# Kernel tuning notes

Measured on AMD Instinct MI355X. Metric: run time of the kernel, lower is better.

Reference implementation:

```python
import math
import jax, jax.numpy as jnp
import numpy as np

MODEL_DIM = 2048
NUM_EXPERTS = 64
NUM_TOKENS = 8192
CAPACITY_FACTOR = 1.0


def setup_inputs() -> dict:
    key = jax.random.key(0)
    kx, kw = jax.random.split(key)
    x = jax.random.normal(kx, (NUM_TOKENS, MODEL_DIM), dtype=jnp.float32)
    # Linear(model_dim, num_experts, bias=False): weight [E, D], y = x @ W.T
    wg = jax.random.normal(kw, (NUM_EXPERTS, MODEL_DIM), dtype=jnp.float32) * (1.0 / math.sqrt(MODEL_DIM))
    return {"x": x, "wg": wg}


def reference(x, wg):
    # ---- gate projection: logits [S, E] ----
    logits = jnp.einsum('sd,ed->se', x, wg)
    gates = jax.nn.softmax(logits, axis=1)
    S, E = gates.shape
    # training mode -> capacity = capacity_factor * ceil(S / E)  (static)
    capacity = int(CAPACITY_FACTOR * math.ceil(S / E))

    # ---- top-1 expert selection ----
    indices1_s = jnp.argmax(gates, axis=1)                      # [S]
    mask1 = jax.nn.one_hot(indices1_s, E, dtype=jnp.int32)      # [S, E]

    # gate value of the chosen expert per token
    gates1_s = jnp.sum(gates * mask1.astype(gates.dtype), axis=1)  # [S]

    # position of each token within its expert's queue (cumsum over tokens)
    locations1 = jnp.cumsum(mask1, axis=0) - 1                  # [S, E]

    # ---- load-balancing auxiliary loss ----
    me = jnp.mean(gates, axis=0)                                # [E]
    ce = jnp.mean(mask1.astype(gates.dtype), axis=0)            # [E]
    l_aux = jnp.mean(me * ce) * (E * E)

    # ---- capacity enforcement: drop tokens beyond expert capacity ----
    mask1 = mask1 * (locations1 < capacity).astype(mask1.dtype) # [S, E]
    locations1_s = jnp.sum(locations1 * mask1, axis=1)          # [S]

    # ---- combine / dispatch tensors ----
    gates1 = gates1_s[:, None] * mask1.astype(gates.dtype)      # [S, E]
    locations1_sc = jax.nn.one_hot(locations1_s, capacity, dtype=gates.dtype)  # [S, C]
    # torch.bmm(gates1[:, :, None], locations1_sc[:, None, :]) == outer product per token
    combine1_sec = jnp.einsum('se,sc->sec', gates1, locations1_sc)  # [S, E, C]
    dispatch_mask = combine1_sec > 0                            # bool [S, E, C]

    return l_aux, combine1_sec, dispatch_mask
```

## Files before the change

kernel.cpp:

```cpp
#include <hip/hip_runtime.h>
#include <math.h>

#define NUM_TOK 8192
#define DIM     2048
#define NEXP    64
#define CAP     128

#define TM      32
#define BK      64
#define NT      256
#define NBLKA   (NUM_TOK/TM)
#define NCHUNK  (DIM/BK)

#define XS_STR  72
#define WS_STR  68
#define LG_STR  (NEXP+1)

#define ZFLT    524288u
#define ZPER    (ZFLT/NCHUNK)

__global__ __launch_bounds__(NT) void gate_fused(
    const float* __restrict__ x, const float* __restrict__ wg,
    float* __restrict__ out,
    int* __restrict__ expert_idx, float* __restrict__ gate_top,
    float* __restrict__ me_partial, int* __restrict__ counts)
{
    __shared__ __align__(16) float xs[TM * XS_STR];
    __shared__ __align__(16) float wss[BK * WS_STR];
    __shared__ __align__(16) float logits_s[TM * LG_STR];
    __shared__ float me_s[NEXP];
    __shared__ int   cnt_s[NEXP];

    const int tid = threadIdx.x;
    const int bid = blockIdx.x;
    const int tx  = tid & 15;
    const int ty  = tid >> 4;
    const int tok0 = bid * TM;

    if (tid < NEXP) { me_s[tid] = 0.0f; cnt_s[tid] = 0; }

    float acc[2][4] = {};

    float* zbase = out + 1 + (size_t)bid * ZFLT;
    const float4 z4 = make_float4(0.f, 0.f, 0.f, 0.f);

    for (int kc = 0; kc < NCHUNK; ++kc) {
        const int k0 = kc * BK;

        {
            float4* zp = (float4*)(zbase + (size_t)kc * ZPER) + tid;
            #pragma unroll
            for (int q = 0; q < 16; ++q) zp[q * NT] = z4;
        }

        #pragma unroll
        for (int q = 0; q < 2; ++q) {
            int id = tid + NT * q;
            int r = id >> 4, cf = id & 15;
            float4 v = *(const float4*)(x + (size_t)(tok0 + r) * DIM + k0 + 4 * cf);
            *(float4*)(&xs[r * XS_STR + 4 * cf]) = v;
        }
        {
            int cf = tid & 15, er = tid >> 4;
            #pragma unroll
            for (int i = 0; i < 4; ++i) {
                int e = er + 16 * i;
                float4 v = *(const float4*)(wg + (size_t)e * DIM + k0 + 4 * cf);
                wss[(4 * cf + 0) * WS_STR + e] = v.x;
                wss[(4 * cf + 1) * WS_STR + e] = v.y;
                wss[(4 * cf + 2) * WS_STR + e] = v.z;
                wss[(4 * cf + 3) * WS_STR + e] = v.w;
            }
        }
        __syncthreads();

        #pragma unroll
        for (int kk = 0; kk < BK; kk += 4) {
            float4 xa = *(const float4*)(&xs[(2 * ty + 0) * XS_STR + kk]);
            float4 xb = *(const float4*)(&xs[(2 * ty + 1) * XS_STR + kk]);
            #pragma unroll
            for (int j = 0; j < 4; ++j) {
                float4 w = *(const float4*)(&wss[(kk + j) * WS_STR + 4 * tx]);
                float xaj = (&xa.x)[j], xbj = (&xb.x)[j];
                acc[0][0] += xaj * w.x; acc[0][1] += xaj * w.y;
                acc[0][2] += xaj * w.z; acc[0][3] += xaj * w.w;
                acc[1][0] += xbj * w.x; acc[1][1] += xbj * w.y;
                acc[1][2] += xbj * w.z; acc[1][3] += xbj * w.w;
            }
        }
        __syncthreads();
    }

    #pragma unroll
    for (int i = 0; i < 2; ++i)
        #pragma unroll
        for (int j = 0; j < 4; ++j)
            logits_s[(2 * ty + i) * LG_STR + 4 * tx + j] = acc[i][j];
    __syncthreads();

    const int lane = tid & 63;
    const int wv   = tid >> 6;
    float me_acc = 0.0f;
    for (int r8 = 0; r8 < 8; ++r8) {
        int row = wv * 8 + r8;
        float v = logits_s[row * LG_STR + lane];
        float m = v; int mi = lane;
        #pragma unroll
        for (int off = 32; off > 0; off >>= 1) {
            float om = __shfl_xor(m, off);
            int  omi = __shfl_xor(mi, off);
            if (om > m || (om == m && omi < mi)) { m = om; mi = omi; }
        }
        float ex = __expf(v - m);
        float s = ex;
        #pragma unroll
        for (int off = 32; off > 0; off >>= 1) s += __shfl_xor(s, off);
        me_acc += ex / s;
        if (lane == mi) {
            int token = tok0 + row;
            expert_idx[token] = mi;
            gate_top[token]   = 1.0f / s;
            atomicAdd(&cnt_s[mi], 1);
        }
    }
    atomicAdd(&me_s[lane], me_acc);
    __syncthreads();
    if (tid < NEXP) {
        me_partial[bid * NEXP + tid] = me_s[tid];
        counts[bid * NEXP + tid]     = cnt_s[tid];
    }
}

__global__ __launch_bounds__(64) void prefix_laux(
    const float* __restrict__ me_partial, const int* __restrict__ counts,
    int* __restrict__ block_off, float* __restrict__ out)
{
    int e = threadIdx.x;
    float me = 0.0f;
    for (int b = 0; b < NBLKA; ++b) me += me_partial[b * NEXP + e];
    int run = 0;
    for (int b = 0; b < NBLKA; ++b) {
        block_off[b * NEXP + e] = run;
        run += counts[b * NEXP + e];
    }
    float ce = (float)run / (float)NUM_TOK;
    me = me / (float)NUM_TOK;
    float v = me * ce;
    #pragma unroll
    for (int off = 32; off > 0; off >>= 1) v += __shfl_xor(v, off);
    if (e == 0) out[0] = v * (float)NEXP;
}

__global__ __launch_bounds__(64) void scatter_k(
    const int* __restrict__ expert_idx, const float* __restrict__ gate_top,
    const int* __restrict__ block_off, float* __restrict__ out)
{
    __shared__ int es[TM];
    int t = threadIdx.x, b = blockIdx.x;
    if (t < TM) es[t] = expert_idx[b * TM + t];
    __syncthreads();
    if (t < TM) {
        int e = es[t];
        int rank = 0;
        for (int u = 0; u < t; ++u) rank += (es[u] == e) ? 1 : 0;
        int loc = block_off[b * NEXP + e] + rank;
        if (loc < CAP) {
            size_t sidx = (size_t)(b * TM + t);
            size_t off  = sidx * (NEXP * CAP) + (size_t)e * CAP + loc;
            out[1 + off] = gate_top[b * TM + t];
            out[1 + (size_t)NUM_TOK * NEXP * CAP + off] = 1.0f;
        }
    }
}

extern "C" void kernel_launch(void* const* d_in, const int* in_sizes, int n_in,
                              void* d_out, int out_size, void* d_ws, size_t ws_size,
                              hipStream_t stream)
{
    const float* x  = (const float*)d_in[0];
    const float* wg = (const float*)d_in[1];
    float* out = (float*)d_out;

    char* ws = (char*)d_ws;
    int*   expert_idx = (int*)  (ws);
    float* gate_top   = (float*)(ws + 32768);
    float* me_partial = (float*)(ws + 65536);
    int*   counts     = (int*)  (ws + 131072);
    int*   block_off  = (int*)  (ws + 196608);

    gate_fused<<<NBLKA, NT, 0, stream>>>(x, wg, out, expert_idx, gate_top,
                                         me_partial, counts);
    prefix_laux<<<1, 64, 0, stream>>>(me_partial, counts, block_off, out);
    scatter_k<<<NBLKA, 64, 0, stream>>>(expert_idx, gate_top, block_off, out);
}
```

Measured before the change: 697.2 us.

## Split zero-fill and GEMM into separate block roles with nontemporal stores

Launches 512 blocks in which even blocks only zero-fill the large combine/dispatch output using nontemporal vector stores, while odd blocks compute the gate GEMM. Each GEMM block stages weight rows in shared memory, and each lane owns one expert for 8 tokens, reading x directly from global memory instead of through shared memory. The per-wave softmax and top-1 selection now work on register accumulators, and shared-memory atomics are replaced with per-wave partial arrays summed at the end. The aim is to overlap the memory-bound zero fill with compute on separate blocks and to avoid write-allocate traffic. The cost is redundant broadcast loads of x from global memory across lanes.

```diff
diff --git a/kernel.cpp b/kernel.cpp
--- a/kernel.cpp
+++ b/kernel.cpp
@@ -1,133 +1,114 @@
 #include <hip/hip_runtime.h>
 #include <math.h>
 
-#define NUM_TOK 8192
 #define DIM     2048
 #define NEXP    64
 #define CAP     128
+#define NTOK    8192
+#define NTILE   256
+#define BKC     128
+#define WROW    132
 
-#define TM      32
-#define BK      64
-#define NT      256
-#define NBLKA   (NUM_TOK/TM)
-#define NCHUNK  (DIM/BK)
+#define OUT_LAST   134217728ull
 
-#define XS_STR  72
-#define WS_STR  68
-#define LG_STR  (NEXP+1)
+typedef float vfloat4 __attribute__((ext_vector_type(4)));
 
-#define ZFLT    524288u
-#define ZPER    (ZFLT/NCHUNK)
-
-__global__ __launch_bounds__(NT) void gate_fused(
+__global__ __launch_bounds__(256) void fused_gate(
     const float* __restrict__ x, const float* __restrict__ wg,
     float* __restrict__ out,
     int* __restrict__ expert_idx, float* __restrict__ gate_top,
     float* __restrict__ me_partial, int* __restrict__ counts)
 {
-    __shared__ __align__(16) float xs[TM * XS_STR];
-    __shared__ __align__(16) float wss[BK * WS_STR];
-    __shared__ __align__(16) float logits_s[TM * LG_STR];
-    __shared__ float me_s[NEXP];
-    __shared__ int   cnt_s[NEXP];
+    __shared__ __align__(16) float wsmem[NEXP * WROW];
+    __shared__ float me_w[4 * NEXP];
+    __shared__ int   cnt_w[4 * NEXP];
 
     const int tid = threadIdx.x;
-    const int bid = blockIdx.x;
-    const int tx  = tid & 15;
-    const int ty  = tid >> 4;
-    const int tok0 = bid * TM;
+    const int b   = blockIdx.x;
 
-    if (tid < NEXP) { me_s[tid] = 0.0f; cnt_s[tid] = 0; }
+    if ((b & 1) == 0) {
+        const int zb = b >> 1;
+        vfloat4* o4 = reinterpret_cast<vfloat4*>(out);
+        const vfloat4 z4 = {0.f, 0.f, 0.f, 0.f};
+        size_t base = (size_t)zb * 131072 + (size_t)tid;
+        #pragma unroll 8
+        for (int q = 0; q < 512; ++q) {
+            size_t i4 = base + ((size_t)q << 8);
+            if (i4 != 0)
+                __builtin_nontemporal_store(z4, &o4[i4]);
+        }
+        if (zb == 0) {
+            if (tid >= 1 && tid <= 3) out[tid] = 0.0f;
+            if (tid == 4) out[OUT_LAST] = 0.0f;
+        }
+        return;
+    }
 
-    float acc[2][4] = {};
+    const int gb   = b >> 1;
+    const int lane = tid & 63;
+    const int wv   = __builtin_amdgcn_readfirstlane(tid >> 6);
+    const int tok0 = gb * 32 + wv * 8;
 
-    float* zbase = out + 1 + (size_t)bid * ZFLT;
-    const float4 z4 = make_float4(0.f, 0.f, 0.f, 0.f);
+    float acc[8] = {};
 
-    for (int kc = 0; kc < NCHUNK; ++kc) {
-        const int k0 = kc * BK;
-
-        {
-            float4* zp = (float4*)(zbase + (size_t)kc * ZPER) + tid;
-            #pragma unroll
-            for (int q = 0; q < 16; ++q) zp[q * NT] = z4;
-        }
-
+    for (int kc = 0; kc < DIM / BKC; ++kc) {
+        const int k0 = kc * BKC;
         #pragma unroll
-        for (int q = 0; q < 2; ++q) {
-            int id = tid + NT * q;
-            int r = id >> 4, cf = id & 15;
-            float4 v = *(const float4*)(x + (size_t)(tok0 + r) * DIM + k0 + 4 * cf);
-            *(float4*)(&xs[r * XS_STR + 4 * cf]) = v;
-        }
-        {
-            int cf = tid & 15, er = tid >> 4;
-            #pragma unroll
-            for (int i = 0; i < 4; ++i) {
-                int e = er + 16 * i;
-                float4 v = *(const float4*)(wg + (size_t)e * DIM + k0 + 4 * cf);
-                wss[(4 * cf + 0) * WS_STR + e] = v.x;
-                wss[(4 * cf + 1) * WS_STR + e] = v.y;
-                wss[(4 * cf + 2) * WS_STR + e] = v.z;
-                wss[(4 * cf + 3) * WS_STR + e] = v.w;
-            }
+        for (int q = 0; q < 8; ++q) {
+            int id = tid + (q << 8);
+            int e  = id >> 5;
+            int c  = id & 31;
+            float4 v = *(const float4*)(wg + (size_t)e * DIM + k0 + (c << 2));
+            *(float4*)(&wsmem[e * WROW + (c << 2)]) = v;
         }
         __syncthreads();
 
-        #pragma unroll
-        for (int kk = 0; kk < BK; kk += 4) {
-            float4 xa = *(const float4*)(&xs[(2 * ty + 0) * XS_STR + kk]);
-            float4 xb = *(const float4*)(&xs[(2 * ty + 1) * XS_STR + kk]);
+        #pragma unroll 4
+        for (int kk = 0; kk < BKC; kk += 4) {
+            float4 w4 = *(const float4*)(&wsmem[lane * WROW + kk]);
             #pragma unroll
-            for (int j = 0; j < 4; ++j) {
-                float4 w = *(const float4*)(&wss[(kk + j) * WS_STR + 4 * tx]);
-                float xaj = (&xa.x)[j], xbj = (&xb.x)[j];
-                acc[0][0] += xaj * w.x; acc[0][1] += xaj * w.y;
-                acc[0][2] += xaj * w.z; acc[0][3] += xaj * w.w;
-                acc[1][0] += xbj * w.x; acc[1][1] += xbj * w.y;
-                acc[1][2] += xbj * w.z; acc[1][3] += xbj * w.w;
+            for (int t = 0; t < 8; ++t) {
+                float4 xv = *(const float4*)(x + (size_t)(tok0 + t) * DIM + k0 + kk);
+                acc[t] = fmaf(xv.x, w4.x, acc[t]);
+                acc[t] = fmaf(xv.y, w4.y, acc[t]);
+                acc[t] = fmaf(xv.z, w4.z, acc[t]);
+                acc[t] = fmaf(xv.w, w4.w, acc[t]);
             }
         }
         __syncthreads();
     }
 
+    float    me_acc  = 0.0f;
+    int      cnt_acc = 0;
     #pragma unroll
-    for (int i = 0; i < 2; ++i)
-        #pragma unroll
-        for (int j = 0; j < 4; ++j)
-            logits_s[(2 * ty + i) * LG_STR + 4 * tx + j] = acc[i][j];
-    __syncthreads();
-
-    const int lane = tid & 63;
-    const int wv   = tid >> 6;
-    float me_acc = 0.0f;
-    for (int r8 = 0; r8 < 8; ++r8) {
-        int row = wv * 8 + r8;
-        float v = logits_s[row * LG_STR + lane];
+    for (int t = 0; t < 8; ++t) {
+        float v = acc[t];
         float m = v; int mi = lane;
         #pragma unroll
         for (int off = 32; off > 0; off >>= 1) {
-            float om = __shfl_xor(m, off);
-            int  omi = __shfl_xor(mi, off);
+            float om  = __shfl_xor(m, off);
+            int   omi = __shfl_xor(mi, off);
             if (om > m || (om == m && omi < mi)) { m = om; mi = omi; }
         }
         float ex = __expf(v - m);
-        float s = ex;
+        float s  = ex;
         #pragma unroll
         for (int off = 32; off > 0; off >>= 1) s += __shfl_xor(s, off);
         me_acc += ex / s;
         if (lane == mi) {
-            int token = tok0 + row;
-            expert_idx[token] = mi;
-            gate_top[token]   = 1.0f / s;
-            atomicAdd(&cnt_s[mi], 1);
+            expert_idx[tok0 + t] = mi;
+            gate_top[tok0 + t]   = 1.0f / s;
+            ++cnt_acc;
         }
     }
-    atomicAdd(&me_s[lane], me_acc);
+    me_w[wv * NEXP + lane]  = me_acc;
+    cnt_w[wv * NEXP + lane] = cnt_acc;
     __syncthreads();
     if (tid < NEXP) {
-        me_partial[bid * NEXP + tid] = me_s[tid];
-        counts[bid * NEXP + tid]     = cnt_s[tid];
+        me_partial[gb * NEXP + tid] = me_w[tid] + me_w[NEXP + tid]
+                                    + me_w[2 * NEXP + tid] + me_w[3 * NEXP + tid];
+        counts[gb * NEXP + tid]     = cnt_w[tid] + cnt_w[NEXP + tid]
+                                    + cnt_w[2 * NEXP + tid] + cnt_w[3 * NEXP + tid];
     }
 }
 
@@ -137,14 +118,14 @@
 {
     int e = threadIdx.x;
     float me = 0.0f;
-    for (int b = 0; b < NBLKA; ++b) me += me_partial[b * NEXP + e];
+    for (int t = 0; t < NTILE; ++t) me += me_partial[t * NEXP + e];
     int run = 0;
-    for (int b = 0; b < NBLKA; ++b) {
-        block_off[b * NEXP + e] = run;
-        run += counts[b * NEXP + e];
+    for (int t = 0; t < NTILE; ++t) {
+        block_off[t * NEXP + e] = run;
+        run += counts[t * NEXP + e];
     }
-    float ce = (float)run / (float)NUM_TOK;
-    me = me / (float)NUM_TOK;
+    float ce = (float)run / (float)NTOK;
+    me = me / (float)NTOK;
     float v = me * ce;
     #pragma unroll
     for (int off = 32; off > 0; off >>= 1) v += __shfl_xor(v, off);
@@ -155,20 +136,20 @@
     const int* __restrict__ expert_idx, const float* __restrict__ gate_top,
     const int* __restrict__ block_off, float* __restrict__ out)
 {
-    __shared__ int es[TM];
+    __shared__ int es[32];
     int t = threadIdx.x, b = blockIdx.x;
-    if (t < TM) es[t] = expert_idx[b * TM + t];
+    if (t < 32) es[t] = expert_idx[b * 32 + t];
     __syncthreads();
-    if (t < TM) {
+    if (t < 32) {
         int e = es[t];
         int rank = 0;
         for (int u = 0; u < t; ++u) rank += (es[u] == e) ? 1 : 0;
         int loc = block_off[b * NEXP + e] + rank;
         if (loc < CAP) {
-            size_t sidx = (size_t)(b * TM + t);
+            size_t sidx = (size_t)(b * 32 + t);
             size_t off  = sidx * (NEXP * CAP) + (size_t)e * CAP + loc;
-            out[1 + off] = gate_top[b * TM + t];
-            out[1 + (size_t)NUM_TOK * NEXP * CAP + off] = 1.0f;
+            out[1 + off] = gate_top[b * 32 + t];
+            out[1 + (size_t)NTOK * NEXP * CAP + off] = 1.0f;
         }
     }
 }
@@ -188,8 +169,8 @@
     int*   counts     = (int*)  (ws + 131072);
     int*   block_off  = (int*)  (ws + 196608);
 
-    gate_fused<<<NBLKA, NT, 0, stream>>>(x, wg, out, expert_idx, gate_top,
-                                         me_partial, counts);
+    fused_gate<<<512, 256, 0, stream>>>(x, wg, out, expert_idx, gate_top,
+                                        me_partial, counts);
     prefix_laux<<<1, 64, 0, stream>>>(me_partial, counts, block_off, out);
-    scatter_k<<<NBLKA, 64, 0, stream>>>(expert_idx, gate_top, block_off, out);
+    scatter_k<<<NTILE, 64, 0, stream>>>(expert_idx, gate_top, block_off, out);
 }
```

Result: slower. 843.1 us (+20.9%).
